# Performance work log

Measured on AMD Instinct MI355X. Metric: run time of the kernel, lower is better.

Reference implementation:

```python
import jax, jax.numpy as jnp
import numpy as np
from jax import lax

B, T_IN, D = 32, 512, 384
F = 384      # x_predictor_filter_size
K = 3        # kernel, padding=1 -> same length
LN_EPS = 1e-5


def setup_inputs() -> dict:
    key = jax.random.key(0)
    ks = jax.random.split(key, 8)
    s = 0.02
    return {
        "x": jax.random.normal(ks[0], (B, T_IN, D), dtype=jnp.float32),
        "target": jax.random.randint(ks[1], (B, T_IN), 0, 8, dtype=jnp.int32),
        "mel_max_length": 4096,
        "conv1_w": jax.random.normal(ks[2], (F, D, K), dtype=jnp.float32) * s,
        "conv1_b": jnp.zeros((F,), jnp.float32),
        "ln1_g": jnp.ones((F,), jnp.float32),
        "ln1_b": jnp.zeros((F,), jnp.float32),
        "conv2_w": jax.random.normal(ks[3], (F, F, K), dtype=jnp.float32) * s,
        "conv2_b": jnp.zeros((F,), jnp.float32),
        "ln2_g": jnp.ones((F,), jnp.float32),
        "ln2_b": jnp.zeros((F,), jnp.float32),
        "lin_w": jax.random.normal(ks[4], (F, 1), dtype=jnp.float32) * s,
        "lin_b": jnp.zeros((1,), jnp.float32),
    }


def _conv1d_same(h_ncl, w, b):
    # h_ncl: [B, C_in, T], w: [C_out, C_in, K], padding=1
    out = lax.conv_general_dilated(h_ncl, w, window_strides=(1,), padding=[(1, 1)],
                                   dimension_numbers=("NCH", "OIH", "NCH"))
    return out + b[None, :, None]


def _layernorm(h, g, b):
    mu = jnp.mean(h, axis=-1, keepdims=True)
    var = jnp.var(h, axis=-1, keepdims=True)
    return (h - mu) * lax.rsqrt(var + LN_EPS) * g + b


def _duration_predictor(x, conv1_w, conv1_b, ln1_g, ln1_b, conv2_w, conv2_b, ln2_g, ln2_b, lin_w, lin_b):
    h = _conv1d_same(jnp.transpose(x, (0, 2, 1)), conv1_w, conv1_b)       # [B,F,T]
    h = jax.nn.relu(_layernorm(jnp.transpose(h, (0, 2, 1)), ln1_g, ln1_b))  # [B,T,F]
    h = _conv1d_same(jnp.transpose(h, (0, 2, 1)), conv2_w, conv2_b)
    h = jax.nn.relu(_layernorm(jnp.transpose(h, (0, 2, 1)), ln2_g, ln2_b))
    return (h @ lin_w + lin_b)[..., 0]  # [B, T_in]


def _length_regulate(x, target, mel_max_length):
    # Equivalent to alignment @ x with one-hot alignment built by create_alignment,
    # expressed as a duration-indexed gather (same math, no dense [B,Tout,Tin]).
    ends = jnp.cumsum(target, axis=1)                 # [B, T_in]
    m = jnp.arange(mel_max_length)                    # [T_out]
    idx = jax.vmap(lambda e: jnp.searchsorted(e, m, side="right"))(ends)  # [B, T_out]
    valid = idx < target.shape[1]                     # frames past total duration -> zero pad
    idx = jnp.minimum(idx, target.shape[1] - 1)
    out = jnp.take_along_axis(x, idx[:, :, None], axis=1)  # [B, T_out, D]
    return out * valid[:, :, None].astype(x.dtype)


def reference(x, target, mel_max_length, conv1_w, conv1_b, ln1_g, ln1_b,
              conv2_w, conv2_b, ln2_g, ln2_b, lin_w, lin_b):
    dur_pred = _duration_predictor(x, conv1_w, conv1_b, ln1_g, ln1_b,
                                   conv2_w, conv2_b, ln2_g, ln2_b, lin_w, lin_b)
    output = _length_regulate(x, target, mel_max_length)
    return output, dur_pred
```

## Files before the change

kernel.cpp:

```cpp
#include <hip/hip_runtime.h>
#include <cstdint>
#include <cstddef>

#define B_   32
#define TIN  512
#define D_   384
#define F_   384
#define TOUT 4096
#define TPAD 514
#define MTOT (B_ * TIN)

typedef __bf16 bf16x8 __attribute__((ext_vector_type(8)));
typedef float  f32x4  __attribute__((ext_vector_type(4)));

__device__ __forceinline__ unsigned short f2bf(float f) {
  unsigned int u = __float_as_uint(f);
  u += 0x7fff + ((u >> 16) & 1);
  return (unsigned short)(u >> 16);
}

__device__ __forceinline__ void load16_to_lds(const void* g, void* l) {
  __builtin_amdgcn_global_load_lds(
      (const __attribute__((address_space(1))) unsigned int*)g,
      (__attribute__((address_space(3))) unsigned int*)l, 16, 0, 0);
}

__global__ void prep_weights(const float* __restrict__ w1, const float* __restrict__ w2,
                             unsigned short* __restrict__ Wt1, unsigned short* __restrict__ Wt2,
                             unsigned short* __restrict__ h1p) {
  int g = blockIdx.x * 256 + threadIdx.x;
  const int WE = 3 * F_ * D_;
  if (g < 2 * WE) {
    int which = g >= WE;
    const float* w = which ? w2 : w1;
    unsigned short* o = which ? Wt2 : Wt1;
    int e = g - which * WE;
    int k = e / (F_ * D_);
    int rem = e - k * (F_ * D_);
    int f = rem / D_;
    int d = rem - f * D_;
    o[e] = f2bf(w[(f * D_ + d) * 3 + k]);
  } else {
    int z = g - 2 * WE;
    int zr = z / D_;
    int c = z - zr * D_;
    int b = zr >> 1;
    int tp = (zr & 1) ? (TPAD - 1) : 0;
    h1p[((size_t)(b * TPAD + tp)) * D_ + c] = 0;
  }
}

__global__ void pad_x(const float4* __restrict__ x4, unsigned short* __restrict__ xp) {
  int g = blockIdx.x * 256 + threadIdx.x;
  int row = g / 96;
  int c4 = g - row * 96;
  int b = row / TPAD;
  int tp = row - b * TPAD;
  ushort4 o;
  if (tp == 0 || tp == TPAD - 1) {
    o.x = 0; o.y = 0; o.z = 0; o.w = 0;
  } else {
    float4 v = x4[((size_t)(b * TIN + tp - 1)) * 96 + c4];
    o.x = f2bf(v.x); o.y = f2bf(v.y); o.z = f2bf(v.z); o.w = f2bf(v.w);
  }
  *(ushort4*)(xp + (size_t)row * D_ + c4 * 4) = o;
}

__global__ __launch_bounds__(256) void conv_gemm(const unsigned short* __restrict__ Ap,
                                                 const unsigned short* __restrict__ Wt,
                                                 const float* __restrict__ bias,
                                                 float* __restrict__ out) {
  __shared__ __align__(16) unsigned short As[128 * 32];
  __shared__ __align__(16) unsigned short Bs[128 * 32];
  const int tid  = threadIdx.x;
  const int wave = tid >> 6;
  const int lane = tid & 63;
  const int quad = lane >> 4;
  const int l15  = lane & 15;
  const int wm = (wave >> 1) * 64;
  const int wn = (wave & 1) * 64;
  const int m0 = blockIdx.x * 128;
  const int n0 = blockIdx.y * 128;
  const int b  = m0 >> 9;
  const int t0 = m0 & 511;

  const int srow = tid >> 2;
  const int scol = (tid & 3) * 8;

  f32x4 acc[4][4];
  for (int i = 0; i < 4; ++i)
    for (int j = 0; j < 4; ++j)
      acc[i][j] = (f32x4){0.f, 0.f, 0.f, 0.f};

  for (int kc = 0; kc < 36; ++kc) {
    int kw = kc / 12;
    int d0 = (kc - kw * 12) * 32;
    for (int r = 0; r < 2; ++r) {
      int row = r * 64 + srow;
      const unsigned short* ga = Ap + (size_t)(b * TPAD + t0 + row + kw) * D_ + d0 + scol;
      load16_to_lds(ga, (char*)As + r * 4096 + wave * 1024);
      const unsigned short* gb = Wt + (size_t)(kw * F_ + n0 + row) * D_ + d0 + scol;
      load16_to_lds(gb, (char*)Bs + r * 4096 + wave * 1024);
    }
    __syncthreads();
    bf16x8 av[4], bv[4];
    for (int mi = 0; mi < 4; ++mi)
      av[mi] = *(const bf16x8*)(As + (wm + mi * 16 + l15) * 32 + quad * 8);
    for (int ni = 0; ni < 4; ++ni)
      bv[ni] = *(const bf16x8*)(Bs + (wn + ni * 16 + l15) * 32 + quad * 8);
    for (int mi = 0; mi < 4; ++mi)
      for (int ni = 0; ni < 4; ++ni)
        acc[mi][ni] = __builtin_amdgcn_mfma_f32_16x16x32_bf16(av[mi], bv[ni], acc[mi][ni], 0, 0, 0);
    __syncthreads();
  }

  for (int mi = 0; mi < 4; ++mi) {
    int mrow = m0 + wm + mi * 16 + quad * 4;
    for (int ni = 0; ni < 4; ++ni) {
      int ncol = n0 + wn + ni * 16 + l15;
      float bb = bias[ncol];
      for (int r = 0; r < 4; ++r)
        out[(size_t)(mrow + r) * F_ + ncol] = acc[mi][ni][r] + bb;
    }
  }
}

__global__ void ln_relu(const float* __restrict__ in, const float* __restrict__ gam,
                        const float* __restrict__ bet, unsigned short* __restrict__ hp) {
  int row = blockIdx.x * 4 + (threadIdx.x >> 6);
  int lane = threadIdx.x & 63;
  const float* p = in + (size_t)row * F_;
  float v[6];
  float s = 0.f, ss = 0.f;
  for (int j = 0; j < 6; ++j) {
    v[j] = p[lane + j * 64];
    s += v[j];
    ss += v[j] * v[j];
  }
  for (int off = 32; off; off >>= 1) {
    s  += __shfl_xor(s, off);
    ss += __shfl_xor(ss, off);
  }
  float mean = s * (1.f / 384.f);
  float var  = ss * (1.f / 384.f) - mean * mean;
  float rstd = rsqrtf(var + 1e-5f);
  int b = row >> 9, t = row & 511;
  unsigned short* o = hp + ((size_t)(b * TPAD + t + 1)) * D_;
  for (int j = 0; j < 6; ++j) {
    int c = lane + j * 64;
    float y = (v[j] - mean) * rstd * gam[c] + bet[c];
    y = y > 0.f ? y : 0.f;
    o[c] = f2bf(y);
  }
}

__global__ void ln_dot(const float* __restrict__ in, const float* __restrict__ gam,
                       const float* __restrict__ bet, const float* __restrict__ lw,
                       const float* __restrict__ lb, float* __restrict__ dur) {
  int row = blockIdx.x * 4 + (threadIdx.x >> 6);
  int lane = threadIdx.x & 63;
  const float* p = in + (size_t)row * F_;
  float v[6];
  float s = 0.f, ss = 0.f;
  for (int j = 0; j < 6; ++j) {
    v[j] = p[lane + j * 64];
    s += v[j];
    ss += v[j] * v[j];
  }
  for (int off = 32; off; off >>= 1) {
    s  += __shfl_xor(s, off);
    ss += __shfl_xor(ss, off);
  }
  float mean = s * (1.f / 384.f);
  float var  = ss * (1.f / 384.f) - mean * mean;
  float rstd = rsqrtf(var + 1e-5f);
  float acc = 0.f;
  for (int j = 0; j < 6; ++j) {
    int c = lane + j * 64;
    float y = (v[j] - mean) * rstd * gam[c] + bet[c];
    y = y > 0.f ? y : 0.f;
    acc += y * lw[c];
  }
  for (int off = 32; off; off >>= 1) acc += __shfl_xor(acc, off);
  if (lane == 0) dur[row] = acc + lb[0];
}

__global__ void cumsum_idx(const int* __restrict__ target, int* __restrict__ idxv) {
  __shared__ int ends[512];
  int t = threadIdx.x, b = blockIdx.x;
  ends[t] = target[b * TIN + t];
  __syncthreads();
  for (int off = 1; off < 512; off <<= 1) {
    int add = (t >= off) ? ends[t - off] : 0;
    __syncthreads();
    ends[t] += add;
    __syncthreads();
  }
  for (int p = 0; p < 8; ++p) {
    int m = p * 512 + t;
    int lo = 0, hi = 512;
    while (lo < hi) {
      int mid = (lo + hi) >> 1;
      if (ends[mid] <= m) lo = mid + 1; else hi = mid;
    }
    idxv[b * TOUT + m] = (lo < TIN) ? lo : -1;
  }
}

__global__ void gather(const float4* __restrict__ x4, const int* __restrict__ idxv,
                       float4* __restrict__ out4) {
  int g = blockIdx.x * 256 + threadIdx.x;
  int fr = g / 96;
  int c = g - fr * 96;
  int id = idxv[fr];
  int b = fr >> 12;
  float4 v = {0.f, 0.f, 0.f, 0.f};
  if (id >= 0) v = x4[(size_t)(b * TIN + id) * 96 + c];
  out4[g] = v;
}

extern "C" void kernel_launch(void* const* d_in, const int* in_sizes, int n_in,
                              void* d_out, int out_size, void* d_ws, size_t ws_size,
                              hipStream_t stream) {
  const float* x      = (const float*)d_in[0];
  const int*   target = (const int*)d_in[1];
  const float* w1  = (const float*)d_in[3];
  const float* b1  = (const float*)d_in[4];
  const float* g1  = (const float*)d_in[5];
  const float* be1 = (const float*)d_in[6];
  const float* w2  = (const float*)d_in[7];
  const float* b2  = (const float*)d_in[8];
  const float* g2  = (const float*)d_in[9];
  const float* be2 = (const float*)d_in[10];
  const float* lw  = (const float*)d_in[11];
  const float* lb  = (const float*)d_in[12];

  float* out = (float*)d_out;
  float* dur = out + (size_t)B_ * TOUT * D_;

  char* ws = (char*)d_ws;
  unsigned short* xp  = (unsigned short*)(ws);
  unsigned short* h1p = (unsigned short*)(ws + 12632064);
  unsigned short* Wt1 = (unsigned short*)(ws + 25264128);
  unsigned short* Wt2 = (unsigned short*)(ws + 26148864);
  float*          gbf = (float*)(ws + 27033600);
  int*            idxv = (int*)(ws + 52199424);

  hipLaunchKernelGGL(prep_weights, dim3(3552), dim3(256), 0, stream, w1, w2, Wt1, Wt2, h1p);
  hipLaunchKernelGGL(pad_x, dim3(6168), dim3(256), 0, stream, (const float4*)x, xp);
  hipLaunchKernelGGL(conv_gemm, dim3(128, 3), dim3(256), 0, stream, xp, Wt1, b1, gbf);
  hipLaunchKernelGGL(ln_relu, dim3(4096), dim3(256), 0, stream, gbf, g1, be1, h1p);
  hipLaunchKernelGGL(conv_gemm, dim3(128, 3), dim3(256), 0, stream, h1p, Wt2, b2, gbf);
  hipLaunchKernelGGL(ln_dot, dim3(4096), dim3(256), 0, stream, gbf, g2, be2, lw, lb, dur);
  hipLaunchKernelGGL(cumsum_idx, dim3(32), dim3(512), 0, stream, target, idxv);
  hipLaunchKernelGGL(gather, dim3(49152), dim3(256), 0, stream, (const float4*)x, idxv, (float4*)out);
}
```

Measured before the change: 331.5 us.

## Merge prep kernels and interleave gather blocks into conv GEMM launches

Folds weight conversion, pad zeroing, x padding and the cumsum/searchsorted index build into one multi-role prep kernel. Splits the memory-bound gather across the two conv GEMM launches by alternating GEMM tiles with gather blocks in one grid, so compute-bound MFMA work overlaps with bandwidth-bound copying. Launch count drops from eight to five. The risk is that gather blocks compete for bandwidth and cache with the GEMM, and mixed block roles can leave the grid imbalanced.

```diff
diff --git a/kernel.cpp b/kernel.cpp
--- a/kernel.cpp
+++ b/kernel.cpp
@@ -25,12 +25,55 @@
       (__attribute__((address_space(3))) unsigned int*)l, 16, 0, 0);
 }
 
-__global__ void prep_weights(const float* __restrict__ w1, const float* __restrict__ w2,
-                             unsigned short* __restrict__ Wt1, unsigned short* __restrict__ Wt2,
-                             unsigned short* __restrict__ h1p) {
-  int g = blockIdx.x * 256 + threadIdx.x;
-  const int WE = 3 * F_ * D_;
-  if (g < 2 * WE) {
+#define PB_CUM 32
+#define PB_W   3456
+#define PB_Z   96
+#define PB_PX  6168
+#define PB_TOT (PB_CUM + PB_W + PB_Z + PB_PX)
+
+__global__ __launch_bounds__(256) void prep_all(
+    const float* __restrict__ w1, const float* __restrict__ w2,
+    unsigned short* __restrict__ Wt1, unsigned short* __restrict__ Wt2,
+    unsigned short* __restrict__ h1p,
+    const int* __restrict__ target, int* __restrict__ idxv,
+    const float4* __restrict__ x4, unsigned short* __restrict__ xp) {
+  int bx = blockIdx.x;
+  int tid = threadIdx.x;
+
+  if (bx < PB_CUM) {
+    __shared__ int ends[512];
+    __shared__ int ps[256];
+    int b = bx;
+    int a0 = target[b * TIN + 2 * tid];
+    int a1 = target[b * TIN + 2 * tid + 1];
+    ps[tid] = a0 + a1;
+    __syncthreads();
+    for (int off = 1; off < 256; off <<= 1) {
+      int add = (tid >= off) ? ps[tid - off] : 0;
+      __syncthreads();
+      ps[tid] += add;
+      __syncthreads();
+    }
+    int incl = ps[tid];
+    ends[2 * tid + 1] = incl;
+    ends[2 * tid]     = incl - a1;
+    __syncthreads();
+    for (int p = 0; p < 16; ++p) {
+      int m = p * 256 + tid;
+      int lo = 0, hi = 512;
+      while (lo < hi) {
+        int mid = (lo + hi) >> 1;
+        if (ends[mid] <= m) lo = mid + 1; else hi = mid;
+      }
+      idxv[b * TOUT + m] = (lo < TIN) ? lo : -1;
+    }
+    return;
+  }
+  bx -= PB_CUM;
+
+  if (bx < PB_W) {
+    int g = bx * 256 + tid;
+    const int WE = 3 * F_ * D_;
     int which = g >= WE;
     const float* w = which ? w2 : w1;
     unsigned short* o = which ? Wt2 : Wt1;
@@ -40,36 +83,42 @@
     int f = rem / D_;
     int d = rem - f * D_;
     o[e] = f2bf(w[(f * D_ + d) * 3 + k]);
-  } else {
-    int z = g - 2 * WE;
+    return;
+  }
+  bx -= PB_W;
+
+  if (bx < PB_Z) {
+    int z = bx * 256 + tid;
     int zr = z / D_;
     int c = z - zr * D_;
     int b = zr >> 1;
     int tp = (zr & 1) ? (TPAD - 1) : 0;
     h1p[((size_t)(b * TPAD + tp)) * D_ + c] = 0;
-  }
-}
-
-__global__ void pad_x(const float4* __restrict__ x4, unsigned short* __restrict__ xp) {
-  int g = blockIdx.x * 256 + threadIdx.x;
-  int row = g / 96;
-  int c4 = g - row * 96;
-  int b = row / TPAD;
-  int tp = row - b * TPAD;
-  ushort4 o;
-  if (tp == 0 || tp == TPAD - 1) {
-    o.x = 0; o.y = 0; o.z = 0; o.w = 0;
-  } else {
-    float4 v = x4[((size_t)(b * TIN + tp - 1)) * 96 + c4];
-    o.x = f2bf(v.x); o.y = f2bf(v.y); o.z = f2bf(v.z); o.w = f2bf(v.w);
-  }
-  *(ushort4*)(xp + (size_t)row * D_ + c4 * 4) = o;
-}
-
-__global__ __launch_bounds__(256) void conv_gemm(const unsigned short* __restrict__ Ap,
-                                                 const unsigned short* __restrict__ Wt,
-                                                 const float* __restrict__ bias,
-                                                 float* __restrict__ out) {
+    return;
+  }
+  bx -= PB_Z;
+
+  {
+    int g = bx * 256 + tid;
+    int row = g / 96;
+    int c4 = g - row * 96;
+    int b = row / TPAD;
+    int tp = row - b * TPAD;
+    ushort4 o;
+    if (tp == 0 || tp == TPAD - 1) {
+      o.x = 0; o.y = 0; o.z = 0; o.w = 0;
+    } else {
+      float4 v = x4[((size_t)(b * TIN + tp - 1)) * 96 + c4];
+      o.x = f2bf(v.x); o.y = f2bf(v.y); o.z = f2bf(v.z); o.w = f2bf(v.w);
+    }
+    *(ushort4*)(xp + (size_t)row * D_ + c4 * 4) = o;
+  }
+}
+
+__device__ __forceinline__ void conv_tile(const unsigned short* __restrict__ Ap,
+                                          const unsigned short* __restrict__ Wt,
+                                          const float* __restrict__ bias,
+                                          float* __restrict__ out, int cb) {
   __shared__ __align__(16) unsigned short As[128 * 32];
   __shared__ __align__(16) unsigned short Bs[128 * 32];
   const int tid  = threadIdx.x;
@@ -79,8 +128,10 @@
   const int l15  = lane & 15;
   const int wm = (wave >> 1) * 64;
   const int wn = (wave & 1) * 64;
-  const int m0 = blockIdx.x * 128;
-  const int n0 = blockIdx.y * 128;
+  const int mt = cb / 3;
+  const int nt = cb - mt * 3;
+  const int m0 = mt * 128;
+  const int n0 = nt * 128;
   const int b  = m0 >> 9;
   const int t0 = m0 & 511;
 
@@ -125,6 +176,29 @@
   }
 }
 
+__global__ __launch_bounds__(256) void conv_gather(
+    const unsigned short* __restrict__ Ap, const unsigned short* __restrict__ Wt,
+    const float* __restrict__ bias, float* __restrict__ out,
+    const float4* __restrict__ x4, const int* __restrict__ idxv,
+    float4* __restrict__ out4, int gpart) {
+  int bx = blockIdx.x;
+  if ((bx & 1) == 0) {
+    conv_tile(Ap, Wt, bias, out, bx >> 1);
+  } else {
+    int gb = gpart * 384 + (bx >> 1);
+    int g = gb * 256 + (int)threadIdx.x;
+    for (int it = 0; it < 64; ++it, g += 768 * 256) {
+      int fr = g / 96;
+      int c = g - fr * 96;
+      int id = idxv[fr];
+      int b = fr >> 12;
+      float4 v = {0.f, 0.f, 0.f, 0.f};
+      if (id >= 0) v = x4[(size_t)(b * TIN + id) * 96 + c];
+      out4[g] = v;
+    }
+  }
+}
+
 __global__ void ln_relu(const float* __restrict__ in, const float* __restrict__ gam,
                         const float* __restrict__ bet, unsigned short* __restrict__ hp) {
   int row = blockIdx.x * 4 + (threadIdx.x >> 6);
@@ -183,40 +257,6 @@
   }
   for (int off = 32; off; off >>= 1) acc += __shfl_xor(acc, off);
   if (lane == 0) dur[row] = acc + lb[0];
-}
-
-__global__ void cumsum_idx(const int* __restrict__ target, int* __restrict__ idxv) {
-  __shared__ int ends[512];
-  int t = threadIdx.x, b = blockIdx.x;
-  ends[t] = target[b * TIN + t];
-  __syncthreads();
-  for (int off = 1; off < 512; off <<= 1) {
-    int add = (t >= off) ? ends[t - off] : 0;
-    __syncthreads();
-    ends[t] += add;
-    __syncthreads();
-  }
-  for (int p = 0; p < 8; ++p) {
-    int m = p * 512 + t;
-    int lo = 0, hi = 512;
-    while (lo < hi) {
-      int mid = (lo + hi) >> 1;
-      if (ends[mid] <= m) lo = mid + 1; else hi = mid;
-    }
-    idxv[b * TOUT + m] = (lo < TIN) ? lo : -1;
-  }
-}
-
-__global__ void gather(const float4* __restrict__ x4, const int* __restrict__ idxv,
-                       float4* __restrict__ out4) {
-  int g = blockIdx.x * 256 + threadIdx.x;
-  int fr = g / 96;
-  int c = g - fr * 96;
-  int id = idxv[fr];
-  int b = fr >> 12;
-  float4 v = {0.f, 0.f, 0.f, 0.f};
-  if (id >= 0) v = x4[(size_t)(b * TIN + id) * 96 + c];
-  out4[g] = v;
 }
 
 extern "C" void kernel_launch(void* const* d_in, const int* in_sizes, int n_in,
@@ -246,12 +286,12 @@
   float*          gbf = (float*)(ws + 27033600);
   int*            idxv = (int*)(ws + 52199424);
 
-  hipLaunchKernelGGL(prep_weights, dim3(3552), dim3(256), 0, stream, w1, w2, Wt1, Wt2, h1p);
-  hipLaunchKernelGGL(pad_x, dim3(6168), dim3(256), 0, stream, (const float4*)x, xp);
-  hipLaunchKernelGGL(conv_gemm, dim3(128, 3), dim3(256), 0, stream, xp, Wt1, b1, gbf);
+  hipLaunchKernelGGL(prep_all, dim3(PB_TOT), dim3(256), 0, stream,
+                     w1, w2, Wt1, Wt2, h1p, target, idxv, (const float4*)x, xp);
+  hipLaunchKernelGGL(conv_gather, dim3(768), dim3(256), 0, stream,
+                     xp, Wt1, b1, gbf, (const float4*)x, idxv, (float4*)out, 0);
   hipLaunchKernelGGL(ln_relu, dim3(4096), dim3(256), 0, stream, gbf, g1, be1, h1p);
-  hipLaunchKernelGGL(conv_gemm, dim3(128, 3), dim3(256), 0, stream, h1p, Wt2, b2, gbf);
+  hipLaunchKernelGGL(conv_gather, dim3(768), dim3(256), 0, stream,
+                     h1p, Wt2, b2, gbf, (const float4*)x, idxv, (float4*)out, 1);
   hipLaunchKernelGGL(ln_dot, dim3(4096), dim3(256), 0, stream, gbf, g2, be2, lw, lb, dur);
-  hipLaunchKernelGGL(cumsum_idx, dim3(32), dim3(512), 0, stream, target, idxv);
-  hipLaunchKernelGGL(gather, dim3(49152), dim3(256), 0, stream, (const float4*)x, idxv, (float4*)out);
-}
+}
```

New measurement: 321.7 us. -2.9%, faster.
